# Optimization experiments

Hardware: AMD Instinct MI355X
Metric: run time of the kernel (lower is better)

The kernel has to match this reference:

```python
import jax, jax.numpy as jnp
import numpy as np

L, N, H = 32768, 256, 256


def _binop(ei, ej):
    a_i, bu_i = ei
    a_j, bu_j = ej
    return (a_j * a_i, a_j * bu_i + bu_j)


def setup_inputs() -> dict:
    key = jax.random.key(0)
    ks = jax.random.split(key, 9)
    # Param values follow init_lru_parameters statistics for numerical sanity.
    u1 = jax.random.uniform(ks[0], (N,), minval=1e-3, maxval=1.0)
    u2 = jax.random.uniform(ks[1], (N,), minval=1e-3, maxval=1.0)
    nu_log = jnp.log(-0.5 * jnp.log(u1))
    theta_log = jnp.log(6.28 * u2)
    B_re = jax.random.normal(ks[2], (N, H)) / np.sqrt(2.0 * H)
    B_im = jax.random.normal(ks[3], (N, H)) / np.sqrt(2.0 * H)
    C_re = jax.random.normal(ks[4], (H, N)) / np.sqrt(1.0 * N)
    C_im = jax.random.normal(ks[5], (H, N)) / np.sqrt(1.0 * N)
    D = jax.random.normal(ks[6], (H,))
    diag_lambda = jnp.exp(-jnp.exp(nu_log) + 1j * jnp.exp(theta_log))
    gamma_log = jnp.log(jnp.sqrt(1.0 - jnp.abs(diag_lambda) ** 2))
    x = jax.random.normal(ks[7], (L, H), dtype=jnp.float32)
    f32 = lambda a: a.astype(jnp.float32)
    return {"x": x, "nu_log": f32(nu_log), "theta_log": f32(theta_log),
            "B_re": f32(B_re), "B_im": f32(B_im), "C_re": f32(C_re),
            "C_im": f32(C_im), "D": f32(D), "gamma_log": f32(gamma_log)}


def reference(x, nu_log, theta_log, B_re, B_im, C_re, C_im, D, gamma_log):
    # Diagonal complex LRU: x_t = Lambda * x_{t-1} + B_norm u_t ; y_t = Re(C x_t) + D*u_t
    Lambda = jnp.exp(-jnp.exp(nu_log) + 1j * jnp.exp(theta_log))        # (N,) complex
    B_norm = (B_re + 1j * B_im) * jnp.exp(gamma_log)[:, None]           # (N,H)
    C = C_re + 1j * C_im                                                # (H,N)
    Bu = x.astype(B_norm.dtype) @ B_norm.T                              # (L,N) complex
    Lam_el = jnp.broadcast_to(Lambda[None, :], Bu.shape)                # (L,N)
    _, states = jax.lax.associative_scan(_binop, (Lam_el, Bu))          # (L,N) complex
    y = (states @ C.T).real + x * D                                     # (L,H) real
    return y
```

## Files before the change

kernel.cpp:

```cpp
#include <hip/hip_runtime.h>

#define L_SEQ 32768
#define NDIM 256
#define HDIM 256
#define NCAT 512
#define LC 64
#define NCHUNK 512

typedef unsigned short u16;
typedef unsigned int u32;
typedef __bf16 bf16x8 __attribute__((ext_vector_type(8)));
typedef float f32x4 __attribute__((ext_vector_type(4)));
typedef __attribute__((address_space(3))) void lds_void;
typedef const __attribute__((address_space(1))) void gbl_void;

__device__ __forceinline__ u16 f2bf(float f) {
  u32 u = __builtin_bit_cast(u32, f);
  u = u + 0x7fffu + ((u >> 16) & 1u);
  return (u16)(u >> 16);
}
__device__ __forceinline__ float bf2f(u16 v) {
  u32 u = ((u32)v) << 16;
  return __builtin_bit_cast(float, u);
}

__global__ __launch_bounds__(256) void prep_kernel(
    const float* __restrict__ x,
    const float* __restrict__ nu_log, const float* __restrict__ theta_log,
    const float* __restrict__ B_re, const float* __restrict__ B_im,
    const float* __restrict__ C_re, const float* __restrict__ C_im,
    const float* __restrict__ gamma_log,
    u16* __restrict__ x_bf, u16* __restrict__ Bcat, u16* __restrict__ Ccat,
    float2* __restrict__ lam, float2* __restrict__ lam64)
{
  const int blk = blockIdx.x, tid = threadIdx.x;
  if (blk < 2048) {
    const float4* src = ((const float4*)x) + (size_t)blk * 1024;
    ushort4* dst = ((ushort4*)x_bf) + (size_t)blk * 1024;
#pragma unroll
    for (int j = 0; j < 4; ++j) {
      float4 v = src[j * 256 + tid];
      dst[j * 256 + tid] = make_ushort4(f2bf(v.x), f2bf(v.y), f2bf(v.z), f2bf(v.w));
    }
  } else if (blk < 2560) {
    int b2 = blk - 2048;
    int jj = b2 >> 1, p = b2 & 1;
    float g = expf(gamma_log[jj]);
    const float* src = (p ? B_im : B_re) + (size_t)jj * HDIM;
    Bcat[(size_t)b2 * HDIM + tid] = f2bf(src[tid] * g);
  } else if (blk < 2816) {
    int h = blk - 2560;
#pragma unroll
    for (int half = 0; half < 2; ++half) {
      int nc = half * 256 + tid;
      int jj = nc >> 1, p = nc & 1;
      float v = p ? -C_im[(size_t)h * NDIM + jj] : C_re[(size_t)h * NDIM + jj];
      Ccat[(size_t)h * NCAT + nc] = f2bf(v);
    }
  } else {
    float nu_e = expf(nu_log[tid]);
    float th = expf(theta_log[tid]);
    float r = expf(-nu_e);
    lam[tid] = make_float2(r * cosf(th), r * sinf(th));
    float r64 = expf(-(float)LC * nu_e);
    float ph = (float)LC * th;
    lam64[tid] = make_float2(r64 * cosf(ph), r64 * sinf(ph));
  }
}

__global__ __launch_bounds__(256) void gemm1_kernel(
    const u16* __restrict__ A,
    const u16* __restrict__ Bm,
    u16* __restrict__ Cout,
    int M, int N, int K)
{
  constexpr int BM = 128, BN = 128, BK = 32;
  __shared__ u16 lA[BM * BK];
  __shared__ u16 lB[BN * BK];
  const int tid = threadIdx.x;
  const int lane = tid & 63, wave = tid >> 6;
  const int bn = blockIdx.x, bm = blockIdx.y;
  const int row0 = bm * BM, col0 = bn * BN;
  const int wm = (wave >> 1) * 64, wn = (wave & 1) * 64;
  const int fr = lane & 15, fo = (lane >> 4) * 8;

  f32x4 acc[4][4] = {};
  const int nkt = K / BK;
  for (int kt = 0; kt < nkt; ++kt) {
    const int k0 = kt * BK;
#pragma unroll
    for (int j = 0; j < 2; ++j) {
      int chunk = j * 256 + tid;
      int r = chunk >> 2, c = chunk & 3;
      const u16* ga = A + (size_t)(row0 + r) * K + (k0 + c * 8);
      const u16* gb = Bm + (size_t)(col0 + r) * K + (k0 + c * 8);
      __builtin_amdgcn_global_load_lds((gbl_void*)ga, (lds_void*)&lA[chunk * 8], 16, 0, 0);
      __builtin_amdgcn_global_load_lds((gbl_void*)gb, (lds_void*)&lB[chunk * 8], 16, 0, 0);
    }
    __syncthreads();

    bf16x8 af[4], bfr[4];
#pragma unroll
    for (int i = 0; i < 4; ++i) {
      af[i]  = *reinterpret_cast<const bf16x8*>(&lA[(wm + i * 16 + fr) * BK + fo]);
      bfr[i] = *reinterpret_cast<const bf16x8*>(&lB[(wn + i * 16 + fr) * BK + fo]);
    }
#pragma unroll
    for (int i = 0; i < 4; ++i)
#pragma unroll
      for (int j = 0; j < 4; ++j)
        acc[i][j] = __builtin_amdgcn_mfma_f32_16x16x32_bf16(af[i], bfr[j], acc[i][j], 0, 0, 0);
    __syncthreads();
  }

  const int fq = lane >> 4;
#pragma unroll
  for (int i = 0; i < 4; ++i)
#pragma unroll
    for (int j = 0; j < 4; ++j) {
      int cg = col0 + wn + j * 16 + fr;
#pragma unroll
      for (int r = 0; r < 4; ++r) {
        int rg = row0 + wm + i * 16 + fq * 4 + r;
        Cout[(size_t)rg * N + cg] = f2bf(acc[i][j][r]);
      }
    }
}

__global__ __launch_bounds__(256) void scan_carry_kernel(
    const ushort2* __restrict__ Bu2, const float2* __restrict__ lam,
    float2* __restrict__ carry)
{
  const int n = threadIdx.x, b = blockIdx.x;
  const float2 la = lam[n];
  float sre = 0.f, sim = 0.f;
  const ushort2* p = Bu2 + (size_t)b * LC * NDIM + n;
#pragma unroll 8
  for (int j = 0; j < LC; ++j) {
    ushort2 bu = p[(size_t)j * NDIM];
    float bre = bf2f(bu.x), bim = bf2f(bu.y);
    float nre = la.x * sre - la.y * sim + bre;
    float nim = la.x * sim + la.y * sre + bim;
    sre = nre; sim = nim;
  }
  carry[(size_t)b * NDIM + n] = make_float2(sre, sim);
}

__global__ __launch_bounds__(512) void carry_scan_kernel(
    const float2* __restrict__ carry, const float2* __restrict__ lam64,
    float2* __restrict__ corr)
{
  __shared__ float4 e[NCHUNK];
  const int n = blockIdx.x;
  const int b = threadIdx.x;
  float2 a = lam64[n];
  float2 v = carry[(size_t)b * NDIM + n];
  e[b] = make_float4(a.x, a.y, v.x, v.y);
  __syncthreads();
#pragma unroll
  for (int d = 1; d < NCHUNK; d <<= 1) {
    float4 prev;
    if (b >= d) prev = e[b - d];
    __syncthreads();
    if (b >= d) {
      float2 ap = make_float2(prev.x, prev.y), vp = make_float2(prev.z, prev.w);
      float2 na, nv;
      na.x = a.x * ap.x - a.y * ap.y;
      na.y = a.x * ap.y + a.y * ap.x;
      nv.x = a.x * vp.x - a.y * vp.y + v.x;
      nv.y = a.x * vp.y + a.y * vp.x + v.y;
      a = na; v = nv;
      e[b] = make_float4(a.x, a.y, v.x, v.y);
    }
    __syncthreads();
  }
  if (b == 0) corr[n] = make_float2(0.f, 0.f);
  if (b < NCHUNK - 1) corr[(size_t)(b + 1) * NDIM + n] = v;
}

__global__ __launch_bounds__(256, 2) void gemm2_kernel(
    const u16* __restrict__ Bu,
    const u16* __restrict__ Cc,
    const float2* __restrict__ lam,
    const float2* __restrict__ corr,
    const u16* __restrict__ xbf,
    const float* __restrict__ Dv,
    float* __restrict__ out)
{
  constexpr int BM = 64, BK = 32, K = NCAT;
  __shared__ u16 sT[BM * K];
  __shared__ u16 lB1[256 * BK];
  const int tid = threadIdx.x;
  const int lane = tid & 63, wave = tid >> 6;
  const int bm = blockIdx.x;
  const int row0 = bm * BM;
  const int wn = wave * 64;
  const int fr = lane & 15, fq = lane >> 4;
  char* sb = (char*)sT;

#pragma unroll
  for (int j = 0; j < 16; ++j) {
    int q = j * 256 + tid;
    int row = q >> 6, off = q & 63;
    const u16* g = Bu + (size_t)(row0 + row) * NCAT + off * 8;
    __builtin_amdgcn_global_load_lds((gbl_void*)g, (lds_void*)&sT[q * 8], 16, 0, 0);
  }
#pragma unroll
  for (int j = 0; j < 4; ++j) {
    int q = j * 256 + tid;
    int row = q >> 2, c = q & 3;
    const u16* g = Cc + (size_t)row * K + c * 8;
    __builtin_amdgcn_global_load_lds((gbl_void*)g, (lds_void*)&lB1[q * 8], 16, 0, 0);
  }
  float2 la = lam[tid];
  float2 c0 = corr[(size_t)bm * NDIM + tid];
  __syncthreads();

  {
    float sre = c0.x, sim = c0.y;
    ushort2 buf[8], nbuf[8];
    const int lb = tid * 4;
#pragma unroll
    for (int s = 0; s < 8; ++s) buf[s] = *(const ushort2*)(sb + s * 1024 + lb);
#pragma unroll
    for (int b8 = 0; b8 < 8; ++b8) {
      if (b8 < 7) {
#pragma unroll
        for (int s = 0; s < 8; ++s)
          nbuf[s] = *(const ushort2*)(sb + (b8 * 8 + 8 + s) * 1024 + lb);
      }
#pragma unroll
      for (int s = 0; s < 8; ++s) {
        int row = b8 * 8 + s;
        float bre = bf2f(buf[s].x), bim = bf2f(buf[s].y);
        float nre = la.x * sre - la.y * sim + bre;
        float nim = la.x * sim + la.y * sre + bim;
        sre = nre; sim = nim;
        *(ushort2*)(sb + row * 1024 + (lb ^ ((row & 7) << 4))) =
            make_ushort2(f2bf(sre), f2bf(sim));
      }
#pragma unroll
      for (int s = 0; s < 8; ++s) buf[s] = nbuf[s];
    }
  }
  __syncthreads();

  f32x4 acc[4][4] = {};
#pragma unroll 1
  for (int kt = 0; kt < 16; ++kt) {
    bf16x8 af[4], bfr[4];
#pragma unroll
    for (int j = 0; j < 4; ++j)
      bfr[j] = *(const bf16x8*)(&lB1[(wn + j * 16 + fr) * BK + fq * 8]);
#pragma unroll
    for (int i = 0; i < 4; ++i) {
      int row = i * 16 + fr;
      int wb = kt * 64 + fq * 16;
      af[i] = *(const bf16x8*)(sb + row * 1024 + (wb ^ ((row & 7) << 4)));
    }
    __syncthreads();
    __builtin_amdgcn_sched_barrier(0);
    if (kt < 15) {
#pragma unroll
      for (int j = 0; j < 4; ++j) {
        int q = j * 256 + tid;
        int row = q >> 2, c = q & 3;
        const u16* g = Cc + (size_t)row * K + (kt + 1) * BK + c * 8;
        __builtin_amdgcn_global_load_lds((gbl_void*)g, (lds_void*)&lB1[q * 8], 16, 0, 0);
      }
    }
    __builtin_amdgcn_sched_barrier(0);
#pragma unroll
    for (int i = 0; i < 4; ++i)
#pragma unroll
      for (int j = 0; j < 4; ++j)
        acc[i][j] = __builtin_amdgcn_mfma_f32_16x16x32_bf16(af[i], bfr[j], acc[i][j], 0, 0, 0);
    __syncthreads();
  }

#pragma unroll
  for (int i = 0; i < 4; ++i)
#pragma unroll
    for (int j = 0; j < 4; ++j) {
      int cg = wn + j * 16 + fr;
      float dvc = Dv[cg];
#pragma unroll
      for (int r = 0; r < 4; ++r) {
        int rg = row0 + i * 16 + fq * 4 + r;
        float v = acc[i][j][r] + bf2f(xbf[(size_t)rg * HDIM + cg]) * dvc;
        out[(size_t)rg * HDIM + cg] = v;
      }
    }
}

extern "C" void kernel_launch(void* const* d_in, const int* in_sizes, int n_in,
                              void* d_out, int out_size, void* d_ws, size_t ws_size,
                              hipStream_t stream)
{
  (void)in_sizes; (void)n_in; (void)out_size; (void)ws_size;
  const float* x         = (const float*)d_in[0];
  const float* nu_log    = (const float*)d_in[1];
  const float* theta_log = (const float*)d_in[2];
  const float* B_re      = (const float*)d_in[3];
  const float* B_im      = (const float*)d_in[4];
  const float* C_re      = (const float*)d_in[5];
  const float* C_im      = (const float*)d_in[6];
  const float* Dv        = (const float*)d_in[7];
  const float* gamma_log = (const float*)d_in[8];

  char* ws = (char*)d_ws;
  u16*    x_bf  = (u16*)ws;
  u16*    Bu_bf = (u16*)(ws + ((size_t)16 << 20));
  u16*    Bcat  = (u16*)(ws + ((size_t)48 << 20));
  u16*    Ccat  = (u16*)(ws + ((size_t)48 << 20) + 262144);
  float2* lam   = (float2*)(ws + ((size_t)48 << 20) + 524288);
  float2* lam64 = (float2*)(ws + ((size_t)48 << 20) + 524288 + 4096);
  float2* carry = (float2*)(ws + ((size_t)49 << 20));
  float2* corr  = (float2*)(ws + ((size_t)50 << 20));

  prep_kernel<<<2817, 256, 0, stream>>>(x, nu_log, theta_log, B_re, B_im,
                                        C_re, C_im, gamma_log,
                                        x_bf, Bcat, Ccat, lam, lam64);

  gemm1_kernel<<<dim3(NCAT / 128, L_SEQ / 128), 256, 0, stream>>>(
      x_bf, Bcat, Bu_bf, L_SEQ, NCAT, HDIM);

  scan_carry_kernel<<<NCHUNK, 256, 0, stream>>>((const ushort2*)Bu_bf, lam, carry);

  carry_scan_kernel<<<NDIM, 512, 0, stream>>>(carry, lam64, corr);

  gemm2_kernel<<<NCHUNK, 256, 0, stream>>>(
      Bu_bf, Ccat, lam, corr, x_bf, Dv, (float*)d_out);
}
```

Baseline: 73.78 us.

## Pre-swizzle B and C weight layouts to avoid LDS bank conflicts in GEMMs

```diff
diff --git a/kernel.cpp b/kernel.cpp
--- a/kernel.cpp
+++ b/kernel.cpp
@@ -43,19 +43,25 @@
       dst[j * 256 + tid] = make_ushort4(f2bf(v.x), f2bf(v.y), f2bf(v.z), f2bf(v.w));
     }
   } else if (blk < 2560) {
-    int b2 = blk - 2048;
-    int jj = b2 >> 1, p = b2 & 1;
+    int pr = blk - 2048;
+    int lr = pr ^ ((pr >> 2) & 1);
+    int jj = lr >> 1, p = lr & 1;
     float g = expf(gamma_log[jj]);
     const float* src = (p ? B_im : B_re) + (size_t)jj * HDIM;
-    Bcat[(size_t)b2 * HDIM + tid] = f2bf(src[tid] * g);
+    int kt = tid >> 5, w = tid & 31, pc = w >> 3, e = w & 7;
+    int lc = kt * 32 + (pc ^ (lr & 3)) * 8 + e;
+    Bcat[(size_t)pr * HDIM + tid] = f2bf(src[lc] * g);
   } else if (blk < 2816) {
-    int h = blk - 2560;
+    int ph = blk - 2560;
+    int lr = ph ^ ((ph >> 2) & 1);
 #pragma unroll
     for (int half = 0; half < 2; ++half) {
-      int nc = half * 256 + tid;
-      int jj = nc >> 1, p = nc & 1;
-      float v = p ? -C_im[(size_t)h * NDIM + jj] : C_re[(size_t)h * NDIM + jj];
-      Ccat[(size_t)h * NCAT + nc] = f2bf(v);
+      int pcol = half * 256 + tid;
+      int kt = pcol >> 5, w = pcol & 31, pc = w >> 3, e = w & 7;
+      int lc2 = kt * 32 + (pc ^ (lr & 3)) * 8 + e;
+      int jj = lc2 >> 1, p = lc2 & 1;
+      float v = p ? -C_im[(size_t)lr * NDIM + jj] : C_re[(size_t)lr * NDIM + jj];
+      Ccat[(size_t)ph * NCAT + pcol] = f2bf(v);
     }
   } else {
     float nu_e = expf(nu_log[tid]);
@@ -82,7 +88,8 @@
   const int bn = blockIdx.x, bm = blockIdx.y;
   const int row0 = bm * BM, col0 = bn * BN;
   const int wm = (wave >> 1) * 64, wn = (wave & 1) * 64;
-  const int fr = lane & 15, fo = (lane >> 4) * 8;
+  const int fr = lane & 15, fq = lane >> 4, fo = fq * 8;
+  const char* lbB = (const char*)lB;
 
   f32x4 acc[4][4] = {};
   const int nkt = K / BK;
@@ -102,8 +109,9 @@
     bf16x8 af[4], bfr[4];
 #pragma unroll
     for (int i = 0; i < 4; ++i) {
-      af[i]  = *reinterpret_cast<const bf16x8*>(&lA[(wm + i * 16 + fr) * BK + fo]);
-      bfr[i] = *reinterpret_cast<const bf16x8*>(&lB[(wn + i * 16 + fr) * BK + fo]);
+      af[i] = *reinterpret_cast<const bf16x8*>(&lA[(wm + i * 16 + fr) * BK + fo]);
+      int rowb = wn + i * 16 + fr;
+      bfr[i] = *(const bf16x8*)(lbB + ((rowb * 64 + fq * 16) ^ ((rowb & 7) << 4)));
     }
 #pragma unroll
     for (int i = 0; i < 4; ++i)
@@ -113,7 +121,6 @@
     __syncthreads();
   }
 
-  const int fq = lane >> 4;
 #pragma unroll
   for (int i = 0; i < 4; ++i)
 #pragma unroll
@@ -197,6 +204,7 @@
   const int wn = wave * 64;
   const int fr = lane & 15, fq = lane >> 4;
   char* sb = (char*)sT;
+  const char* cbB = (const char*)lB1;
 
 #pragma unroll
   for (int j = 0; j < 16; ++j) {
@@ -250,8 +258,10 @@
   for (int kt = 0; kt < 16; ++kt) {
     bf16x8 af[4], bfr[4];
 #pragma unroll
-    for (int j = 0; j < 4; ++j)
-      bfr[j] = *(const bf16x8*)(&lB1[(wn + j * 16 + fr) * BK + fq * 8]);
+    for (int j = 0; j < 4; ++j) {
+      int rowb = wn + j * 16 + fr;
+      bfr[j] = *(const bf16x8*)(cbB + ((rowb * 64 + fq * 16) ^ ((rowb & 7) << 4)));
+    }
 #pragma unroll
     for (int i = 0; i < 4; ++i) {
       int row = i * 16 + fr;
```

Result: no change. 73.76 us (-0.0%).
